# Optimization experiments

Hardware: AMD Instinct MI355X
Metric: run time of the kernel (lower is better)

The kernel has to match this reference:

```python
import jax, jax.numpy as jnp
import numpy as np

D_MODEL = 1024
N_HEADS = 16
FACTOR = 2
KEY_DIM = D_MODEL // N_HEADS            # 64
HEAD_DIM = D_MODEL * FACTOR // N_HEADS  # 128
SCALING = KEY_DIM ** -0.5
BSZ, SEQ = 2, 2048


def _rel_pos(slen):
    # angle: 1/10000**linspace(0,1,key_dim//2), each value repeated twice
    half = jnp.asarray(1.0) / jnp.power(10000.0, jnp.linspace(0.0, 1.0, KEY_DIM // 2))
    angle = jnp.repeat(half, 2)                              # [key_dim]
    decay = jnp.log(1.0 - 2.0 ** (-5.0 - jnp.arange(N_HEADS, dtype=jnp.float32)))  # [h], negative
    idx = jnp.arange(slen, dtype=jnp.float32)
    sin = jnp.sin(idx[:, None] * angle[None, :])             # [s, key_dim]
    cos = jnp.cos(idx[:, None] * angle[None, :])
    diff = idx[:, None] - idx[None, :]                       # [s, s]
    tril = diff >= 0
    mask = jnp.where(tril[None], jnp.exp(diff[None] * decay[:, None, None]), 0.0)  # [h, s, s]
    mask = mask / jnp.sqrt(mask.sum(axis=-1, keepdims=True))
    return sin, cos, mask


def _rotate_every_two(x):
    x1 = x[..., ::2]
    x2 = x[..., 1::2]
    return jnp.stack((-x2, x1), axis=-1).reshape(x.shape)


def _theta_shift(x, sin, cos):
    return x * cos + _rotate_every_two(x) * sin


def setup_inputs() -> dict:
    key = jax.random.key(0)
    ks = jax.random.split(key, 11)
    s = 1.0 / np.sqrt(D_MODEL)
    s2 = 1.0 / np.sqrt(D_MODEL * FACTOR)
    return {
        "x": jax.random.normal(ks[0], (BSZ, SEQ, D_MODEL), jnp.float32),
        "q_w": jax.random.uniform(ks[1], (D_MODEL, D_MODEL), jnp.float32, -s, s),
        "q_b": jax.random.uniform(ks[2], (D_MODEL,), jnp.float32, -s, s),
        "k_w": jax.random.uniform(ks[3], (D_MODEL, D_MODEL), jnp.float32, -s, s),
        "k_b": jax.random.uniform(ks[4], (D_MODEL,), jnp.float32, -s, s),
        "v_w": jax.random.uniform(ks[5], (D_MODEL, D_MODEL * FACTOR), jnp.float32, -s, s),
        "v_b": jax.random.uniform(ks[6], (D_MODEL * FACTOR,), jnp.float32, -s, s),
        "g_w": jax.random.uniform(ks[7], (D_MODEL, D_MODEL * FACTOR), jnp.float32, -s, s),
        "g_b": jax.random.uniform(ks[8], (D_MODEL * FACTOR,), jnp.float32, -s, s),
        "o_w": jax.random.uniform(ks[9], (D_MODEL * FACTOR, D_MODEL), jnp.float32, -s2, s2),
        "o_b": jax.random.uniform(ks[10], (D_MODEL,), jnp.float32, -s2, s2),
    }


def _forward(x, q_w, q_b, k_w, k_b, v_w, v_b, g_w, g_b, o_w, o_b):
    bsz, slen, _ = x.shape
    sin, cos, mask = _rel_pos(slen)
    q = x @ q_w + q_b
    k = (x @ k_w + k_b) * SCALING
    v = x @ v_w + v_b
    g = x @ g_w + g_b
    # [b, h, s, key_dim]
    q = q.reshape(bsz, slen, N_HEADS, KEY_DIM).transpose(0, 2, 1, 3)
    k = k.reshape(bsz, slen, N_HEADS, KEY_DIM).transpose(0, 2, 1, 3)
    qr = _theta_shift(q, sin, cos)
    kr = _theta_shift(k, sin, cos)
    vr = v.reshape(bsz, slen, N_HEADS, HEAD_DIM).transpose(0, 2, 1, 3)  # [b,h,s,head_dim]
    qk = jnp.einsum('bhmd,bhnd->bhmn', qr, kr) * mask                  # decay-masked scores
    denom = jnp.clip(jnp.abs(jax.lax.stop_gradient(qk).sum(axis=-1, keepdims=True)), 1.0, None)
    qk = qk / denom
    out = jnp.einsum('bhmn,bhnd->bhmd', qk, vr).transpose(0, 2, 1, 3)  # [b,s,h,head_dim]
    # per-head LayerNorm over head_dim, no affine
    mu = out.mean(axis=-1, keepdims=True)
    var = out.var(axis=-1, keepdims=True)
    out = (out - mu) / jnp.sqrt(var + 1e-5)
    out = out.reshape(bsz, slen, N_HEADS * HEAD_DIM)
    out = jax.nn.silu(g) * out
    return out @ o_w + o_b


def reference(x, q_w, q_b, k_w, k_b, v_w, v_b, g_w, g_b, o_w, o_b):
    return _forward(x, q_w, q_b, k_w, k_b, v_w, v_b, g_w, g_b, o_w, o_b)
```

## Files before the change

### kernel.cpp

```cpp
#include <hip/hip_runtime.h>
#include <hip/hip_bf16.h>


typedef __hip_bfloat16 bf16;
typedef short bf16x4 __attribute__((ext_vector_type(4)));
typedef short bf16x8 __attribute__((ext_vector_type(8)));
typedef float floatx4 __attribute__((ext_vector_type(4)));

#define B_SZ 2
#define SEQ 2048
#define NH 16
#define KD 64
#define HD 128

#define ASYNC16(gp, lp)                                                             \
  __builtin_amdgcn_global_load_lds(                                                 \
      (const __attribute__((address_space(1))) unsigned int*)(unsigned long long)(const void*)(gp), \
      (__attribute__((address_space(3))) unsigned int*)(unsigned int)(unsigned long long)(void*)(lp), \
      16, 0, 0)

__device__ __forceinline__ float b2f(bf16 x) { return __bfloat162float(x); }
__device__ __forceinline__ bf16 f2b(float x) { return __float2bfloat16(x); }

__global__ void convert_k(const float* __restrict__ in, bf16* __restrict__ out) {
  int i = blockIdx.x * 256 + threadIdx.x;
  float4 v = reinterpret_cast<const float4*>(in)[i];
  union { bf16 h[4]; bf16x4 v4; } u;
  u.h[0] = f2b(v.x); u.h[1] = f2b(v.y); u.h[2] = f2b(v.z); u.h[3] = f2b(v.w);
  reinterpret_cast<bf16x4*>(out)[i] = u.v4;
}

__global__ void transpose_k(const float* __restrict__ in, bf16* __restrict__ out,
                            int K, int N) {
  __shared__ float tile[32][33];
  int tx = threadIdx.x, ty = threadIdx.y;
  int n0 = blockIdx.x * 32, k0 = blockIdx.y * 32;
#pragma unroll
  for (int j = 0; j < 4; ++j)
    tile[ty + j * 8][tx] = in[(size_t)(k0 + ty + j * 8) * N + n0 + tx];
  __syncthreads();
#pragma unroll
  for (int j = 0; j < 4; ++j)
    out[(size_t)(n0 + ty + j * 8) * K + k0 + tx] = f2b(tile[tx][ty + j * 8]);
}

template <int BM, int BN, int KDIM, int MODE>
__global__ __launch_bounds__(256, 2) void gemm_bt(
    const bf16* __restrict__ A, const bf16* __restrict__ Bt, int Ndim,
    const float* __restrict__ bias_q, const float* __restrict__ bias_k,
    const float* __restrict__ bias_v, const float* __restrict__ bias_g,
    float* __restrict__ outCqk, bf16* __restrict__ out_vT,
    float* __restrict__ out_g, float* __restrict__ outF) {
  __shared__ bf16 As[BM * 32];
  __shared__ bf16 Bs[BN * 32];
  const int tid = threadIdx.x;
  const int wave = tid >> 6, lane = tid & 63;
  const int quad = lane >> 4, l16 = lane & 15;
  const int m0 = blockIdx.y * BM, n0 = blockIdx.x * BN;
  constexpr int FI = BM / 32;
  constexpr int FJ = BN / 32;
  const int wm = (wave >> 1) * (BM / 2), wn = (wave & 1) * (BN / 2);

  floatx4 acc[FI][FJ] = {};

  for (int k0 = 0; k0 < KDIM; k0 += 32) {
#pragma unroll
    for (int j = 0; j < BM / 64; ++j) {
      int cbase = (j * 4 + wave) * 64;
      int c = cbase + lane;
      const bf16* g = A + (size_t)(m0 + (c >> 2)) * KDIM + k0 + (c & 3) * 8;
      ASYNC16(g, &As[cbase * 8]);
    }
#pragma unroll
    for (int j = 0; j < BN / 64; ++j) {
      int cbase = (j * 4 + wave) * 64;
      int c = cbase + lane;
      const bf16* g = Bt + (size_t)(n0 + (c >> 2)) * KDIM + k0 + (c & 3) * 8;
      ASYNC16(g, &Bs[cbase * 8]);
    }
    __syncthreads();

    bf16x8 af[FI], bfr[FJ];
#pragma unroll
    for (int i = 0; i < FI; ++i)
      af[i] = *(const bf16x8*)&As[(wm + i * 16 + l16) * 32 + quad * 8];
#pragma unroll
    for (int j = 0; j < FJ; ++j)
      bfr[j] = *(const bf16x8*)&Bs[(wn + j * 16 + l16) * 32 + quad * 8];
#pragma unroll
    for (int i = 0; i < FI; ++i)
#pragma unroll
      for (int j = 0; j < FJ; ++j)
        acc[i][j] = __builtin_amdgcn_mfma_f32_16x16x32_bf16(af[i], bfr[j],
                                                            acc[i][j], 0, 0, 0);
    __syncthreads();
  }

#pragma unroll
  for (int i = 0; i < FI; ++i) {
#pragma unroll
    for (int j = 0; j < FJ; ++j) {
#pragma unroll
      for (int r = 0; r < 4; ++r) {
        int gm = m0 + wm + i * 16 + quad * 4 + r;
        int gn = n0 + wn + j * 16 + l16;
        float v = acc[i][j][r];
        if (MODE == 1) {
          v += bias_q[gn];
          outF[(size_t)gm * Ndim + gn] = v;
        } else {
          int b = gm >> 11, s = gm & 2047;
          if (gn < 2048) {
            bool is_k = gn >= 1024;
            int jj = is_k ? gn - 1024 : gn;
            v += is_k ? bias_k[jj] : bias_q[jj];
            if (is_k) v *= 0.125f;
            outCqk[(size_t)gm * 2048 + gn] = v;
          } else if (gn < 4096) {
            int jj = gn - 2048;
            v += bias_v[jj];
            int h = jj >> 7, d = jj & 127;
            out_vT[(((size_t)b * NH + h) * HD + d) * SEQ + s] = f2b(v);
          } else {
            int jj = gn - 4096;
            v += bias_g[jj];
            out_g[(size_t)gm * 2048 + jj] = v;
          }
        }
      }
    }
  }
}

__global__ void router_k(const float* __restrict__ Cqk,
                         bf16* __restrict__ qh, bf16* __restrict__ ql,
                         bf16* __restrict__ kh, bf16* __restrict__ kl) {
  int t = blockIdx.x * 256 + threadIdx.x;
  int row = t >> 10, pc = t & 1023;
  int b = row >> 11, s = row & 2047;
  bool is_k = pc >= 512;
  int jj = (pc - (is_k ? 512 : 0)) * 2;
  int h = jj >> 6, d = jj & 63, ii = d >> 1;
  float2 v = *(const float2*)&Cqk[(size_t)row * 2048 + pc * 2];
  float half = exp2f(-(float)ii * (13.287712379549449f / 31.0f));
  float ang = (float)s * half;
  float sn = sinf(ang), cs = cosf(ang);
  float e = v.x * cs - v.y * sn;
  float o = v.y * cs + v.x * sn;
  bf16 eh = f2b(e), oh = f2b(o);
  bf16 el = f2b(e - b2f(eh)), ol = f2b(o - b2f(oh));
  size_t idx = (((size_t)b * NH + h) * SEQ + s) * KD + d;
  bf16* ph = is_k ? kh : qh;
  bf16* pl = is_k ? kl : ql;
  union { bf16 h2[2]; unsigned u; } uh, ul;
  uh.h2[0] = eh; uh.h2[1] = oh;
  ul.h2[0] = el; ul.h2[1] = ol;
  *(unsigned*)&ph[idx] = uh.u;
  *(unsigned*)&pl[idx] = ul.u;
}

__global__ __launch_bounds__(256, 4) void retention_k(
    const bf16* __restrict__ qh, const bf16* __restrict__ ql,
    const bf16* __restrict__ kh, const bf16* __restrict__ kl,
    const bf16* __restrict__ vT, const float* __restrict__ g,
    bf16* __restrict__ gated) {
  __shared__ bf16 KHs[32 * 64];
  __shared__ bf16 KLs[32 * 64];
  __shared__ bf16 Vs[128 * 32];
  __shared__ bf16 Pl[4][16 * 32];
  const int tid = threadIdx.x;
  const int wave = tid >> 6, lane = tid & 63;
  const int quad = lane >> 4, l16 = lane & 15;
  const int h = blockIdx.y, b = blockIdx.z;
  const int bh = b * NH + h;
  const int bt = 31 - blockIdx.x;
  const int m0 = bt * 64 + wave * 16;
  const int ntiles = 2 * bt + 2;

  const float t = exp2f(-(float)(5 + h));
  const float lng = log1pf(-t);
  const float log2g = lng * 1.44269504088896340736f;

  float rf[4];
#pragma unroll
  for (int r = 0; r < 4; ++r) {
    int m = m0 + quad * 4 + r;
    float num = -expm1f((float)(m + 1) * lng);
    rf[r] = exp2f((float)m * log2g) * rsqrtf(num / t);
  }
  const float gstep = exp2f(-32.0f * log2g);
  const float cf0 = exp2f(-(float)l16 * log2g);
  const float cf1 = cf0 * exp2f(-16.0f * log2g);

  const size_t qoff = ((size_t)bh * SEQ + m0 + l16) * KD;
  bf16x8 aq0h = *(const bf16x8*)&qh[qoff + quad * 8];
  bf16x8 aq1h = *(const bf16x8*)&qh[qoff + 32 + quad * 8];
  bf16x8 aq0l = *(const bf16x8*)&ql[qoff + quad * 8];
  bf16x8 aq1l = *(const bf16x8*)&ql[qoff + 32 + quad * 8];

  floatx4 oacc[8] = {};
  float rowsum[4] = {0.f, 0.f, 0.f, 0.f};

  const bf16* khb = kh + (size_t)bh * SEQ * KD;
  const bf16* klb = kl + (size_t)bh * SEQ * KD;
  const bf16* vbase = vT + (size_t)bh * HD * SEQ;

  for (int nt = 0; nt < ntiles; ++nt) {
    const int n0 = nt * 32;

#pragma unroll
    for (int j = 0; j < 4; ++j) {
      int cc = wave * 4 + j;
      if (cc < 8) {
        const bf16* src = (cc < 4) ? khb : klb;
        bf16* dst = (cc < 4) ? KHs : KLs;
        int r = ((cc & 3) * 8) + (lane >> 3);
        int s = lane & 7;
        int q = (s - r) & 7;
        const bf16* gp = src + (size_t)(n0 + r) * KD + q * 8;
        ASYNC16(gp, &dst[(cc & 3) * 512]);
      } else {
        int r = (cc - 8) * 16 + (lane >> 2);
        int s = lane & 3;
        int q = (s - (r >> 1)) & 3;
        const bf16* gp = vbase + (size_t)r * SEQ + n0 + q * 8;
        ASYNC16(gp, &Vs[(cc - 8) * 512]);
      }
    }
    __syncthreads();

    const bool active = (n0 <= m0 + 15);
    if (active) {
      floatx4 sc[2];
#pragma unroll
      for (int hh = 0; hh < 2; ++hh) {
        int krow = hh * 16 + l16;
        int c0 = ((quad + krow) & 7) * 8;
        int c1 = ((quad + 4 + krow) & 7) * 8;
        bf16x8 bkh0 = *(const bf16x8*)&KHs[krow * 64 + c0];
        bf16x8 bkh1 = *(const bf16x8*)&KHs[krow * 64 + c1];
        bf16x8 bkl0 = *(const bf16x8*)&KLs[krow * 64 + c0];
        bf16x8 bkl1 = *(const bf16x8*)&KLs[krow * 64 + c1];
        floatx4 z1 = {0.f, 0.f, 0.f, 0.f}, z2 = z1, z3 = z1;
        z1 = __builtin_amdgcn_mfma_f32_16x16x32_bf16(aq0h, bkh0, z1, 0, 0, 0);
        z2 = __builtin_amdgcn_mfma_f32_16x16x32_bf16(aq0l, bkh0, z2, 0, 0, 0);
        z3 = __builtin_amdgcn_mfma_f32_16x16x32_bf16(aq0h, bkl0, z3, 0, 0, 0);
        z1 = __builtin_amdgcn_mfma_f32_16x16x32_bf16(aq1h, bkh1, z1, 0, 0, 0);
        z2 = __builtin_amdgcn_mfma_f32_16x16x32_bf16(aq1l, bkh1, z2, 0, 0, 0);
        z3 = __builtin_amdgcn_mfma_f32_16x16x32_bf16(aq1h, bkl1, z3, 0, 0, 0);
        sc[hh] = z1 + z2 + z3;
      }

#pragma unroll
      for (int hh = 0; hh < 2; ++hh) {
        float cf = hh ? cf1 : cf0;
#pragma unroll
        for (int r = 0; r < 4; ++r) {
          int m = m0 + quad * 4 + r;
          int n = n0 + hh * 16 + l16;
          float p = (m >= n) ? sc[hh][r] * rf[r] * cf : 0.f;
          rowsum[r] += p;
          Pl[wave][(quad * 4 + r) * 32 + hh * 16 + l16] = f2b(p);
        }
      }
#pragma unroll
      for (int r = 0; r < 4; ++r) rf[r] *= gstep;

      asm volatile("s_waitcnt lgkmcnt(0)" ::: "memory");
      bf16x8 pa = *(const bf16x8*)&Pl[wave][l16 * 32 + quad * 8];

#pragma unroll
      for (int dt = 0; dt < 8; ++dt) {
        int vrow = dt * 16 + l16;
        bf16x8 bv = *(const bf16x8*)&Vs[vrow * 32 + ((quad + (vrow >> 1)) & 3) * 8];
        oacc[dt] = __builtin_amdgcn_mfma_f32_16x16x32_bf16(pa, bv, oacc[dt], 0, 0, 0);
      }
    }
    __syncthreads();
  }

  float inv_den[4];
#pragma unroll
  for (int r = 0; r < 4; ++r) {
    float v = rowsum[r];
    v += __shfl_xor(v, 1);
    v += __shfl_xor(v, 2);
    v += __shfl_xor(v, 4);
    v += __shfl_xor(v, 8);
    inv_den[r] = 1.0f / fmaxf(fabsf(v), 1.0f);
  }
  float s1[4] = {}, s2[4] = {};
#pragma unroll
  for (int dt = 0; dt < 8; ++dt) {
#pragma unroll
    for (int r = 0; r < 4; ++r) {
      float v = oacc[dt][r] * inv_den[r];
      oacc[dt][r] = v;
      s1[r] += v;
      s2[r] += v * v;
    }
  }
  float mean[4], istd[4];
#pragma unroll
  for (int r = 0; r < 4; ++r) {
    float a = s1[r], q2 = s2[r];
    a += __shfl_xor(a, 1); a += __shfl_xor(a, 2);
    a += __shfl_xor(a, 4); a += __shfl_xor(a, 8);
    q2 += __shfl_xor(q2, 1); q2 += __shfl_xor(q2, 2);
    q2 += __shfl_xor(q2, 4); q2 += __shfl_xor(q2, 8);
    mean[r] = a * (1.0f / 128.0f);
    float var = q2 * (1.0f / 128.0f) - mean[r] * mean[r];
    istd[r] = rsqrtf(fmaxf(var, 0.0f) + 1e-5f);
  }
#pragma unroll
  for (int dt = 0; dt < 8; ++dt) {
#pragma unroll
    for (int r = 0; r < 4; ++r) {
      int m = m0 + quad * 4 + r;
      int col = h * HD + dt * 16 + l16;
      float v = (oacc[dt][r] - mean[r]) * istd[r];
      float gv = g[((size_t)b * SEQ + m) * 2048 + col];
      float sg = gv / (1.0f + expf(-gv));
      gated[((size_t)b * SEQ + m) * 2048 + col] = f2b(sg * v);
    }
  }
}

extern "C" void kernel_launch(void* const* d_in, const int* in_sizes, int n_in,
                              void* d_out, int out_size, void* d_ws,
                              size_t ws_size, hipStream_t stream) {
  const float* x   = (const float*)d_in[0];
  const float* q_w = (const float*)d_in[1];
  const float* q_b = (const float*)d_in[2];
  const float* k_w = (const float*)d_in[3];
  const float* k_b = (const float*)d_in[4];
  const float* v_w = (const float*)d_in[5];
  const float* v_b = (const float*)d_in[6];
  const float* g_w = (const float*)d_in[7];
  const float* g_b = (const float*)d_in[8];
  const float* o_w = (const float*)d_in[9];
  const float* o_b = (const float*)d_in[10];

  char* ws = (char*)d_ws;
  bf16* Wt    = (bf16*)ws; ws += (size_t)6144 * 1024 * 2;
  bf16* oT    = (bf16*)ws; ws += (size_t)1024 * 2048 * 2;
  bf16* xb    = (bf16*)ws; ws += (size_t)4096 * 1024 * 2;
  float* Cqk  = (float*)ws; ws += (size_t)4096 * 2048 * 4;
  bf16* qhb   = (bf16*)ws; ws += (size_t)32 * 2048 * 64 * 2;
  bf16* qlb   = (bf16*)ws; ws += (size_t)32 * 2048 * 64 * 2;
  bf16* khb   = (bf16*)ws; ws += (size_t)32 * 2048 * 64 * 2;
  bf16* klb   = (bf16*)ws; ws += (size_t)32 * 2048 * 64 * 2;
  bf16* vTb   = (bf16*)ws; ws += (size_t)32 * 128 * 2048 * 2;
  float* gbuf = (float*)ws; ws += (size_t)2 * 2048 * 2048 * 4;
  bf16* gated = (bf16*)ws; ws += (size_t)4096 * 2048 * 2;

  convert_k<<<(4096 * 1024 / 4) / 256, 256, 0, stream>>>(x, xb);

  dim3 tb(32, 8);
  transpose_k<<<dim3(1024 / 32, 1024 / 32), tb, 0, stream>>>(q_w, Wt, 1024, 1024);
  transpose_k<<<dim3(1024 / 32, 1024 / 32), tb, 0, stream>>>(k_w, Wt + (size_t)1024 * 1024, 1024, 1024);
  transpose_k<<<dim3(2048 / 32, 1024 / 32), tb, 0, stream>>>(v_w, Wt + (size_t)2048 * 1024, 1024, 2048);
  transpose_k<<<dim3(2048 / 32, 1024 / 32), tb, 0, stream>>>(g_w, Wt + (size_t)4096 * 1024, 1024, 2048);
  transpose_k<<<dim3(1024 / 32, 2048 / 32), tb, 0, stream>>>(o_w, oT, 2048, 1024);

  gemm_bt<128, 128, 1024, 0><<<dim3(6144 / 128, 4096 / 128), 256, 0, stream>>>(
      xb, Wt, 6144, q_b, k_b, v_b, g_b, Cqk, vTb, gbuf, nullptr);

  router_k<<<(4096 * 1024) / 256, 256, 0, stream>>>(Cqk, qhb, qlb, khb, klb);

  retention_k<<<dim3(32, NH, B_SZ), 256, 0, stream>>>(
      qhb, qlb, khb, klb, vTb, gbuf, gated);

  gemm_bt<128, 64, 2048, 1><<<dim3(1024 / 64, 4096 / 128), 256, 0, stream>>>(
      gated, oT, 1024, o_b, nullptr, nullptr, nullptr, nullptr, nullptr,
      nullptr, (float*)d_out);
}
```

Baseline: 379.4 us.

## Double-buffer retention K/V tiles and stage V transpose through a separate kernel

The retention kernel now double-buffers its K-high, K-low and V tiles in LDS. It prefetches the next tile with async global-to-LDS loads while computing on the current one, which drops the trailing barrier per iteration. Separately, the projection GEMM now writes V row-major into a scratch buffer that aliases the gated buffer. A new tiled transpose kernel then produces the per-head V^T layout, replacing the scattered strided bf16 stores in the GEMM epilogue. The costs are double the LDS use per block, which may reduce occupancy, and an extra kernel launch plus an extra read/write pass over V.

Result: no change. 372.2 us (-1.9%).

```diff
diff --git a/kernel.cpp b/kernel.cpp
--- a/kernel.cpp
+++ b/kernel.cpp
@@ -44,12 +44,27 @@
     out[(size_t)(n0 + ty + j * 8) * K + k0 + tx] = f2b(tile[tx][ty + j * 8]);
 }
 
+__global__ void vtrans_k(const bf16* __restrict__ in, bf16* __restrict__ out) {
+  __shared__ bf16 tile[32][34];
+  int tx = threadIdx.x, ty = threadIdx.y;
+  int s0 = blockIdx.x * 32, c0 = blockIdx.y * 32;
+  const bf16* src = in + (size_t)blockIdx.z * 2048 * 2048;
+  bf16* dst = out + (size_t)blockIdx.z * 2048 * 2048;
+#pragma unroll
+  for (int j = 0; j < 4; ++j)
+    tile[ty + j * 8][tx] = src[(size_t)(s0 + ty + j * 8) * 2048 + c0 + tx];
+  __syncthreads();
+#pragma unroll
+  for (int j = 0; j < 4; ++j)
+    dst[(size_t)(c0 + ty + j * 8) * 2048 + s0 + tx] = tile[tx][ty + j * 8];
+}
+
 template <int BM, int BN, int KDIM, int MODE>
 __global__ __launch_bounds__(256, 2) void gemm_bt(
     const bf16* __restrict__ A, const bf16* __restrict__ Bt, int Ndim,
     const float* __restrict__ bias_q, const float* __restrict__ bias_k,
     const float* __restrict__ bias_v, const float* __restrict__ bias_g,
-    float* __restrict__ outCqk, bf16* __restrict__ out_vT,
+    float* __restrict__ outCqk, bf16* __restrict__ out_v,
     float* __restrict__ out_g, float* __restrict__ outF) {
   __shared__ bf16 As[BM * 32];
   __shared__ bf16 Bs[BN * 32];
@@ -109,7 +124,6 @@
           v += bias_q[gn];
           outF[(size_t)gm * Ndim + gn] = v;
         } else {
-          int b = gm >> 11, s = gm & 2047;
           if (gn < 2048) {
             bool is_k = gn >= 1024;
             int jj = is_k ? gn - 1024 : gn;
@@ -119,8 +133,7 @@
           } else if (gn < 4096) {
             int jj = gn - 2048;
             v += bias_v[jj];
-            int h = jj >> 7, d = jj & 127;
-            out_vT[(((size_t)b * NH + h) * HD + d) * SEQ + s] = f2b(v);
+            out_v[(size_t)gm * 2048 + jj] = f2b(v);
           } else {
             int jj = gn - 4096;
             v += bias_g[jj];
@@ -164,9 +177,9 @@
     const bf16* __restrict__ kh, const bf16* __restrict__ kl,
     const bf16* __restrict__ vT, const float* __restrict__ g,
     bf16* __restrict__ gated) {
-  __shared__ bf16 KHs[32 * 64];
-  __shared__ bf16 KLs[32 * 64];
-  __shared__ bf16 Vs[128 * 32];
+  __shared__ bf16 KHs[2][32 * 64];
+  __shared__ bf16 KLs[2][32 * 64];
+  __shared__ bf16 Vs[2][128 * 32];
   __shared__ bf16 Pl[4][16 * 32];
   const int tid = threadIdx.x;
   const int wave = tid >> 6, lane = tid & 63;
@@ -205,29 +218,37 @@
   const bf16* klb = kl + (size_t)bh * SEQ * KD;
   const bf16* vbase = vT + (size_t)bh * HD * SEQ;
 
-  for (int nt = 0; nt < ntiles; ++nt) {
-    const int n0 = nt * 32;
-
+  auto stage = [&](int nt, int buf) {
+    const int n0s = nt * 32;
 #pragma unroll
     for (int j = 0; j < 4; ++j) {
       int cc = wave * 4 + j;
       if (cc < 8) {
         const bf16* src = (cc < 4) ? khb : klb;
-        bf16* dst = (cc < 4) ? KHs : KLs;
+        bf16* dst = (cc < 4) ? KHs[buf] : KLs[buf];
         int r = ((cc & 3) * 8) + (lane >> 3);
         int s = lane & 7;
         int q = (s - r) & 7;
-        const bf16* gp = src + (size_t)(n0 + r) * KD + q * 8;
-        ASYNC16(gp, &dst[(cc & 3) * 512]);
+        ASYNC16(src + (size_t)(n0s + r) * KD + q * 8, &dst[(cc & 3) * 512]);
       } else {
         int r = (cc - 8) * 16 + (lane >> 2);
         int s = lane & 3;
         int q = (s - (r >> 1)) & 3;
-        const bf16* gp = vbase + (size_t)r * SEQ + n0 + q * 8;
-        ASYNC16(gp, &Vs[(cc - 8) * 512]);
+        ASYNC16(vbase + (size_t)r * SEQ + n0s + q * 8, &Vs[buf][(cc - 8) * 512]);
       }
     }
+  };
+
+  stage(0, 0);
+  for (int nt = 0; nt < ntiles; ++nt) {
+    const int n0 = nt * 32;
+    const int cur = nt & 1;
+    asm volatile("s_waitcnt vmcnt(0) lgkmcnt(0)" ::: "memory");
     __syncthreads();
+    {
+      int pf = (nt + 1 < ntiles) ? nt + 1 : nt;
+      stage(pf, cur ^ 1);
+    }
 
     const bool active = (n0 <= m0 + 15);
     if (active) {
@@ -237,10 +258,10 @@
         int krow = hh * 16 + l16;
         int c0 = ((quad + krow) & 7) * 8;
         int c1 = ((quad + 4 + krow) & 7) * 8;
-        bf16x8 bkh0 = *(const bf16x8*)&KHs[krow * 64 + c0];
-        bf16x8 bkh1 = *(const bf16x8*)&KHs[krow * 64 + c1];
-        bf16x8 bkl0 = *(const bf16x8*)&KLs[krow * 64 + c0];
-        bf16x8 bkl1 = *(const bf16x8*)&KLs[krow * 64 + c1];
+        bf16x8 bkh0 = *(const bf16x8*)&KHs[cur][krow * 64 + c0];
+        bf16x8 bkh1 = *(const bf16x8*)&KHs[cur][krow * 64 + c1];
+        bf16x8 bkl0 = *(const bf16x8*)&KLs[cur][krow * 64 + c0];
+        bf16x8 bkl1 = *(const bf16x8*)&KLs[cur][krow * 64 + c1];
         floatx4 z1 = {0.f, 0.f, 0.f, 0.f}, z2 = z1, z3 = z1;
         z1 = __builtin_amdgcn_mfma_f32_16x16x32_bf16(aq0h, bkh0, z1, 0, 0, 0);
         z2 = __builtin_amdgcn_mfma_f32_16x16x32_bf16(aq0l, bkh0, z2, 0, 0, 0);
@@ -272,11 +293,10 @@
 #pragma unroll
       for (int dt = 0; dt < 8; ++dt) {
         int vrow = dt * 16 + l16;
-        bf16x8 bv = *(const bf16x8*)&Vs[vrow * 32 + ((quad + (vrow >> 1)) & 3) * 8];
+        bf16x8 bv = *(const bf16x8*)&Vs[cur][vrow * 32 + ((quad + (vrow >> 1)) & 3) * 8];
         oacc[dt] = __builtin_amdgcn_mfma_f32_16x16x32_bf16(pa, bv, oacc[dt], 0, 0, 0);
       }
     }
-    __syncthreads();
   }
 
   float inv_den[4];
@@ -353,6 +373,7 @@
   bf16* vTb   = (bf16*)ws; ws += (size_t)32 * 128 * 2048 * 2;
   float* gbuf = (float*)ws; ws += (size_t)2 * 2048 * 2048 * 4;
   bf16* gated = (bf16*)ws; ws += (size_t)4096 * 2048 * 2;
+  bf16* vbuf  = gated;
 
   convert_k<<<(4096 * 1024 / 4) / 256, 256, 0, stream>>>(x, xb);
 
@@ -364,7 +385,9 @@
   transpose_k<<<dim3(1024 / 32, 2048 / 32), tb, 0, stream>>>(o_w, oT, 2048, 1024);
 
   gemm_bt<128, 128, 1024, 0><<<dim3(6144 / 128, 4096 / 128), 256, 0, stream>>>(
-      xb, Wt, 6144, q_b, k_b, v_b, g_b, Cqk, vTb, gbuf, nullptr);
+      xb, Wt, 6144, q_b, k_b, v_b, g_b, Cqk, vbuf, gbuf, nullptr);
+
+  vtrans_k<<<dim3(64, 64, B_SZ), tb, 0, stream>>>(vbuf, vTb);
 
   router_k<<<(4096 * 1024) / 256, 256, 0, stream>>>(Cqk, qhb, qlb, khb, klb);
 
```
